# Performance work log

Hardware: AMD Instinct MI355X
Metric: run time of the kernel (lower is better)

Reference implementation:

```python
import jax, jax.numpy as jnp
import numpy as np

N, H, E = 40000, 128, 640000
BN_EPS = 1e-5


def setup_inputs() -> dict:
    key = jax.random.key(0)
    ks = jax.random.split(key, 5)
    x = jax.random.normal(ks[0], (N, H), dtype=jnp.float32)
    edge_index = jax.random.randint(ks[1], (2, E), 0, N, dtype=jnp.int64)
    eps = jnp.zeros((1,), dtype=jnp.float32)
    s = 1.0 / np.sqrt(H)  # torch Linear init scale
    W1 = jax.random.uniform(ks[2], (H, H), jnp.float32, -s, s)
    b1 = jnp.zeros((H,), dtype=jnp.float32)
    W2 = jax.random.uniform(ks[3], (H, H), jnp.float32, -s, s)
    b2 = jnp.zeros((H,), dtype=jnp.float32)
    gamma = jnp.ones((H,), dtype=jnp.float32)
    beta = jnp.zeros((H,), dtype=jnp.float32)
    return {"x": x, "edge_index": edge_index, "eps": eps,
            "W1": W1, "b1": b1, "W2": W2, "b2": b2,
            "gamma": gamma, "beta": beta}


def reference(x, edge_index, eps, W1, b1, W2, b2, gamma, beta):
    src = edge_index[0]
    tgt = edge_index[1]
    # gather source features, scatter-add into target rows: [N, H]
    agg = jax.ops.segment_sum(x[src], tgt, num_segments=x.shape[0])
    out = agg + (1.0 + eps) * x
    # MLP: Linear -> ReLU -> Linear -> BatchNorm1d (train mode) -> ReLU
    h = jax.nn.relu(out @ W1.T + b1)
    h = h @ W2.T + b2
    mean = jnp.mean(h, axis=0)
    var = jnp.mean((h - mean) ** 2, axis=0)  # biased var, as BN uses
    h = (h - mean) * jax.lax.rsqrt(var + BN_EPS) * gamma + beta
    return jax.nn.relu(h)
```

## Files before the change

### kernel.cpp

```cpp
#include <hip/hip_runtime.h>

#define HDIM 128
#define BN_EPS 1e-5f
#define SCAN_BINS 1024
#define NPART 8
#define LSTR 136

typedef short short8 __attribute__((ext_vector_type(8)));
typedef float floatx4 __attribute__((ext_vector_type(4)));

__device__ __forceinline__ unsigned short f2b(float f) {
    union { float f; unsigned u; } v; v.f = f;
    unsigned r = v.u + 0x7FFFu + ((v.u >> 16) & 1u);
    return (unsigned short)(r >> 16);
}

__device__ __forceinline__ float b2f(unsigned short b) {
    union { unsigned u; float f; } v; v.u = (unsigned)b << 16;
    return v.f;
}

__global__ __launch_bounds__(256) void prep_kernel(
    const float* __restrict__ x, unsigned short* __restrict__ xB, long n4,
    const float* __restrict__ W1, const float* __restrict__ W2,
    unsigned short* __restrict__ W1B, unsigned short* __restrict__ W2B,
    const int* __restrict__ eidx, int* __restrict__ hist, int E)
{
    int tid = blockIdx.x * 256 + threadIdx.x;
    int stride = gridDim.x * 256;
    for (long i = tid; i < n4; i += stride) {
        float4 v = ((const float4*)x)[i];
        ushort4 o;
        o.x = f2b(v.x); o.y = f2b(v.y); o.z = f2b(v.z); o.w = f2b(v.w);
        ((ushort4*)xB)[i] = o;
    }
    for (int i = tid; i < HDIM * HDIM; i += stride) {
        W1B[i] = f2b(W1[i]);
        W2B[i] = f2b(W2[i]);
    }
    for (int e = tid; e < E; e += stride) {
        atomicAdd(&hist[eidx[E + e]], 1);
    }
}

__global__ __launch_bounds__(256) void block_scan_kernel(
    const int* __restrict__ hist, int* __restrict__ offsets,
    int* __restrict__ blockSums, float* __restrict__ statSum, int N)
{
    __shared__ int ts[256];
    int b = blockIdx.x, t = threadIdx.x;
    if (b == 0 && t < 2 * HDIM) statSum[t] = 0.f;
    int base = b * SCAN_BINS + t * 4;
    int4 h = make_int4(0, 0, 0, 0);
    if (base + 3 < N) {
        h = *(const int4*)(hist + base);
    } else {
        if (base + 0 < N) h.x = hist[base + 0];
        if (base + 1 < N) h.y = hist[base + 1];
        if (base + 2 < N) h.z = hist[base + 2];
    }
    int s = h.x + h.y + h.z + h.w;
    ts[t] = s;
    __syncthreads();
    for (int off = 1; off < 256; off <<= 1) {
        int v = ts[t];
        int add = (t >= off) ? ts[t - off] : 0;
        __syncthreads();
        ts[t] = v + add;
        __syncthreads();
    }
    int excl = ts[t] - s;
    int4 o;
    o.x = excl;
    o.y = o.x + h.x;
    o.z = o.y + h.y;
    o.w = o.z + h.z;
    if (base + 3 < N) {
        *(int4*)(offsets + base) = o;
    } else {
        if (base + 0 < N) offsets[base + 0] = o.x;
        if (base + 1 < N) offsets[base + 1] = o.y;
        if (base + 2 < N) offsets[base + 2] = o.z;
    }
    if (t == 255) blockSums[b] = ts[255];
}

__global__ __launch_bounds__(256) void scan_finalize_kernel(
    const int* __restrict__ blockSums, int* __restrict__ offsets,
    int* __restrict__ cursor, int N, int NB)
{
    __shared__ int ts[256];
    int b = blockIdx.x, t = threadIdx.x;
    ts[t] = (t < NB) ? blockSums[t] : 0;
    __syncthreads();
    for (int off = 1; off < 256; off <<= 1) {
        int v = ts[t];
        int add = (t >= off) ? ts[t - off] : 0;
        __syncthreads();
        ts[t] = v + add;
        __syncthreads();
    }
    int prefix = (b == 0) ? 0 : ts[b - 1];
    if (b == 0 && t == 0) offsets[N] = ts[NB - 1];
    int base = b * SCAN_BINS + t * 4;
    if (base + 3 < N) {
        int4 o = *(int4*)(offsets + base);
        o.x += prefix; o.y += prefix; o.z += prefix; o.w += prefix;
        *(int4*)(offsets + base) = o;
        *(int4*)(cursor + base) = o;
    } else {
        for (int j = 0; j < 4; j++) {
            int i = base + j;
            if (i < N) {
                int v = offsets[i] + prefix;
                offsets[i] = v;
                cursor[i] = v;
            }
        }
    }
}

__global__ __launch_bounds__(256) void reorder_kernel(
    const int* __restrict__ eidx, int* __restrict__ cursor,
    int* __restrict__ srcSorted, int E, int partSize)
{
    int part = blockIdx.x & (NPART - 1);
    int bi = blockIdx.x >> 3;
    int nb = gridDim.x >> 3;
    int lo = part * partSize;
    int hi = lo + partSize;
    int stride = nb * 256;
    for (int e = bi * 256 + threadIdx.x; e < E; e += stride) {
        int t = eidx[E + e];
        if (t >= lo && t < hi) {
            int pos = atomicAdd(&cursor[t], 1);
            srcSorted[pos] = eidx[e];
        }
    }
}

__global__ __launch_bounds__(256, 6) void mega_kernel(
    const float* __restrict__ x, const unsigned short* __restrict__ xB,
    const int* __restrict__ offsets, const int* __restrict__ srcSorted,
    const float* __restrict__ eps,
    const unsigned short* __restrict__ W1B, const float* __restrict__ b1,
    const unsigned short* __restrict__ W2B, const float* __restrict__ b2,
    float* __restrict__ out, float* __restrict__ statSum,
    float* __restrict__ statSqs, int N)
{
    __shared__ unsigned short sT[64 * LSTR];
    __shared__ float sSum[HDIM];
    __shared__ float sSqs[HDIM];

    int tid = threadIdx.x;
    int rb = blockIdx.x * 64;
    if (tid < HDIM) { sSum[tid] = 0.f; sSqs[tid] = 0.f; }

    float coef = 1.0f + eps[0];
    int tx = tid & 15, ty = tid >> 4;
    for (int g = 0; g < 4; g++) {
        int r = g * 16 + ty;
        int row = rb + r;
        int col = tx * 8;
        float acc[8] = {0.f, 0.f, 0.f, 0.f, 0.f, 0.f, 0.f, 0.f};
        if (row < N) {
            float4 xv0 = *(const float4*)(x + (size_t)row * HDIM + col);
            float4 xv1 = *(const float4*)(x + (size_t)row * HDIM + col + 4);
            acc[0] = coef * xv0.x; acc[1] = coef * xv0.y;
            acc[2] = coef * xv0.z; acc[3] = coef * xv0.w;
            acc[4] = coef * xv1.x; acc[5] = coef * xv1.y;
            acc[6] = coef * xv1.z; acc[7] = coef * xv1.w;
            int beg = offsets[row], end = offsets[row + 1];
            int e = beg;
            for (; e + 3 < end; e += 4) {
                int s0 = srcSorted[e];
                int s1 = srcSorted[e + 1];
                int s2 = srcSorted[e + 2];
                int s3 = srcSorted[e + 3];
                short8 u0 = *(const short8*)(xB + (size_t)s0 * HDIM + col);
                short8 u1 = *(const short8*)(xB + (size_t)s1 * HDIM + col);
                short8 u2 = *(const short8*)(xB + (size_t)s2 * HDIM + col);
                short8 u3 = *(const short8*)(xB + (size_t)s3 * HDIM + col);
                #pragma unroll
                for (int j = 0; j < 8; j++)
                    acc[j] += (b2f((unsigned short)u0[j]) + b2f((unsigned short)u1[j]))
                            + (b2f((unsigned short)u2[j]) + b2f((unsigned short)u3[j]));
            }
            for (; e < end; e++) {
                int s = srcSorted[e];
                short8 u = *(const short8*)(xB + (size_t)s * HDIM + col);
                #pragma unroll
                for (int j = 0; j < 8; j++)
                    acc[j] += b2f((unsigned short)u[j]);
            }
        }
        short8 o;
        #pragma unroll
        for (int j = 0; j < 8; j++) o[j] = (short)f2b(acc[j]);
        *(short8*)(sT + r * LSTR + col) = o;
    }
    __syncthreads();

    int w = tid >> 6;
    int l = tid & 63;
    int m = l & 15, quad = l >> 4;
    unsigned short* myT = sT + w * 16 * LSTR;

    floatx4 acc1[8];
    #pragma unroll
    for (int t = 0; t < 8; t++) acc1[t] = (floatx4){0.f, 0.f, 0.f, 0.f};
    #pragma unroll
    for (int kk = 0; kk < 4; kk++) {
        int k0 = kk * 32 + quad * 8;
        short8 a = *(const short8*)(myT + m * LSTR + k0);
        #pragma unroll
        for (int t = 0; t < 8; t++) {
            short8 bfr = *(const short8*)(W1B + (size_t)(t * 16 + m) * HDIM + k0);
            acc1[t] = __builtin_amdgcn_mfma_f32_16x16x32_bf16(a, bfr, acc1[t], 0, 0, 0);
        }
    }
    #pragma unroll
    for (int t = 0; t < 8; t++) {
        int col = t * 16 + m;
        float bs = b1[col];
        #pragma unroll
        for (int r = 0; r < 4; r++) {
            float v = fmaxf(acc1[t][r] + bs, 0.f);
            myT[(quad * 4 + r) * LSTR + col] = f2b(v);
        }
    }

    floatx4 acc2[8];
    #pragma unroll
    for (int t = 0; t < 8; t++) acc2[t] = (floatx4){0.f, 0.f, 0.f, 0.f};
    #pragma unroll
    for (int kk = 0; kk < 4; kk++) {
        int k0 = kk * 32 + quad * 8;
        short8 a = *(const short8*)(myT + m * LSTR + k0);
        #pragma unroll
        for (int t = 0; t < 8; t++) {
            short8 bfr = *(const short8*)(W2B + (size_t)(t * 16 + m) * HDIM + k0);
            acc2[t] = __builtin_amdgcn_mfma_f32_16x16x32_bf16(a, bfr, acc2[t], 0, 0, 0);
        }
    }
    int row0 = rb + w * 16 + quad * 4;
    #pragma unroll
    for (int t = 0; t < 8; t++) {
        int col = t * 16 + m;
        float bs = b2[col];
        float cs = 0.f, cq = 0.f;
        #pragma unroll
        for (int r = 0; r < 4; r++) {
            int row = row0 + r;
            if (row < N) {
                float v = acc2[t][r] + bs;
                out[(size_t)row * HDIM + col] = v;
                cs += v; cq += v * v;
            }
        }
        cs += __shfl_xor(cs, 16, 64);
        cs += __shfl_xor(cs, 32, 64);
        cq += __shfl_xor(cq, 16, 64);
        cq += __shfl_xor(cq, 32, 64);
        if (quad == 0) {
            atomicAdd(&sSum[col], cs);
            atomicAdd(&sSqs[col], cq);
        }
    }
    __syncthreads();
    if (tid < HDIM) {
        atomicAdd(&statSum[tid], sSum[tid]);
        atomicAdd(&statSqs[tid], sSqs[tid]);
    }
}

__global__ __launch_bounds__(256) void bn_apply_kernel(
    float* __restrict__ out, const float* __restrict__ statSum,
    const float* __restrict__ statSqs, const float* __restrict__ gamma,
    const float* __restrict__ beta, int N, long n4)
{
    __shared__ float sSc[HDIM];
    __shared__ float sSh[HDIM];
    int t = threadIdx.x;
    if (t < HDIM) {
        float invN = 1.0f / (float)N;
        float mean = statSum[t] * invN;
        float var = statSqs[t] * invN - mean * mean;
        float sc = gamma[t] * rsqrtf(var + BN_EPS);
        sSc[t] = sc;
        sSh[t] = beta[t] - mean * sc;
    }
    __syncthreads();
    long stride = (long)gridDim.x * 256;
    for (long i = (long)blockIdx.x * 256 + t; i < n4; i += stride) {
        int cg = (int)(i & 31) * 4;
        float4 v = ((float4*)out)[i];
        v.x = fmaxf(v.x * sSc[cg + 0] + sSh[cg + 0], 0.f);
        v.y = fmaxf(v.y * sSc[cg + 1] + sSh[cg + 1], 0.f);
        v.z = fmaxf(v.z * sSc[cg + 2] + sSh[cg + 2], 0.f);
        v.w = fmaxf(v.w * sSc[cg + 3] + sSh[cg + 3], 0.f);
        ((float4*)out)[i] = v;
    }
}

extern "C" void kernel_launch(void* const* d_in, const int* in_sizes, int n_in,
                              void* d_out, int out_size, void* d_ws, size_t ws_size,
                              hipStream_t stream) {
    const float* x     = (const float*)d_in[0];
    const int*   eidx  = (const int*)d_in[1];
    const float* eps   = (const float*)d_in[2];
    const float* W1    = (const float*)d_in[3];
    const float* b1    = (const float*)d_in[4];
    const float* W2    = (const float*)d_in[5];
    const float* b2    = (const float*)d_in[6];
    const float* gamma = (const float*)d_in[7];
    const float* beta  = (const float*)d_in[8];
    float* out = (float*)d_out;

    int N = in_sizes[0] / HDIM;
    int E = in_sizes[1] / 2;
    size_t NH = (size_t)N * HDIM;
    int NB = (N + SCAN_BINS - 1) / SCAN_BINS;
    int NpadOff = (N + 1 + 3) & ~3;
    int partSize = (N + NPART - 1) / NPART;
    long n4 = (long)NH / 4;

    unsigned short* xB   = (unsigned short*)d_ws;
    unsigned short* W1B  = xB + NH;
    unsigned short* W2B  = W1B + HDIM * HDIM;
    float* statSum = (float*)(W2B + HDIM * HDIM);
    float* statSqs = statSum + HDIM;
    int*   hist    = (int*)(statSqs + HDIM);
    int*   offsets = hist + N;
    int*   cursor  = offsets + NpadOff;
    int*   srcSorted = cursor + N;
    int*   blockSums = srcSorted + E;

    hipMemsetAsync(hist, 0, (size_t)N * sizeof(int), stream);
    prep_kernel<<<1280, 256, 0, stream>>>(x, xB, n4, W1, W2, W1B, W2B, eidx, hist, E);
    block_scan_kernel<<<NB, 256, 0, stream>>>(hist, offsets, blockSums, statSum, N);
    scan_finalize_kernel<<<NB, 256, 0, stream>>>(blockSums, offsets, cursor, N, NB);
    reorder_kernel<<<2048, 256, 0, stream>>>(eidx, cursor, srcSorted, E, partSize);
    int gblocks = (N + 63) / 64;
    mega_kernel<<<gblocks, 256, 0, stream>>>(
        x, xB, offsets, srcSorted, eps, W1B, b1, W2B, b2,
        out, statSum, statSqs, N);
    bn_apply_kernel<<<2048, 256, 0, stream>>>(
        out, statSum, statSqs, gamma, beta, N, n4);
}
```

Before: 215.8 us.

## Split edge gather across two half-warps and halve rows per block

Each block now handles 32 rows instead of 64. Each destination row's edge list is split between two 16-lane halves, which interleave edges and combine their partial sums with a cross-lane shuffle. The MLP stage splits the output columns across wave pairs, so each wave computes 16 rows by 64 columns, with an extra barrier and a separate shared buffer for the hidden activations. The aim is more memory-level parallelism in the gather and more blocks in flight. The cost is more blocks, more per-block atomics for the batch-norm statistics, and each wave reloading the weight fragments.

```diff
diff --git a/kernel.cpp b/kernel.cpp
--- a/kernel.cpp
+++ b/kernel.cpp
@@ -148,35 +148,33 @@
     float* __restrict__ out, float* __restrict__ statSum,
     float* __restrict__ statSqs, int N)
 {
-    __shared__ unsigned short sT[64 * LSTR];
+    __shared__ unsigned short sAgg[32 * LSTR];
+    __shared__ unsigned short sH[32 * LSTR];
     __shared__ float sSum[HDIM];
     __shared__ float sSqs[HDIM];
 
     int tid = threadIdx.x;
-    int rb = blockIdx.x * 64;
+    int rb = blockIdx.x * 32;
     if (tid < HDIM) { sSum[tid] = 0.f; sSqs[tid] = 0.f; }
 
     float coef = 1.0f + eps[0];
-    int tx = tid & 15, ty = tid >> 4;
+    int lane32 = tid & 31;
+    int colgrp = lane32 & 15;
+    int half = lane32 >> 4;
+    int rp = tid >> 5;
+    int col = colgrp * 8;
     for (int g = 0; g < 4; g++) {
-        int r = g * 16 + ty;
+        int r = g * 8 + rp;
         int row = rb + r;
-        int col = tx * 8;
         float acc[8] = {0.f, 0.f, 0.f, 0.f, 0.f, 0.f, 0.f, 0.f};
         if (row < N) {
-            float4 xv0 = *(const float4*)(x + (size_t)row * HDIM + col);
-            float4 xv1 = *(const float4*)(x + (size_t)row * HDIM + col + 4);
-            acc[0] = coef * xv0.x; acc[1] = coef * xv0.y;
-            acc[2] = coef * xv0.z; acc[3] = coef * xv0.w;
-            acc[4] = coef * xv1.x; acc[5] = coef * xv1.y;
-            acc[6] = coef * xv1.z; acc[7] = coef * xv1.w;
             int beg = offsets[row], end = offsets[row + 1];
-            int e = beg;
-            for (; e + 3 < end; e += 4) {
+            int e = beg + half;
+            for (; e + 6 < end; e += 8) {
                 int s0 = srcSorted[e];
-                int s1 = srcSorted[e + 1];
-                int s2 = srcSorted[e + 2];
-                int s3 = srcSorted[e + 3];
+                int s1 = srcSorted[e + 2];
+                int s2 = srcSorted[e + 4];
+                int s3 = srcSorted[e + 6];
                 short8 u0 = *(const short8*)(xB + (size_t)s0 * HDIM + col);
                 short8 u1 = *(const short8*)(xB + (size_t)s1 * HDIM + col);
                 short8 u2 = *(const short8*)(xB + (size_t)s2 * HDIM + col);
@@ -186,75 +184,94 @@
                     acc[j] += (b2f((unsigned short)u0[j]) + b2f((unsigned short)u1[j]))
                             + (b2f((unsigned short)u2[j]) + b2f((unsigned short)u3[j]));
             }
-            for (; e < end; e++) {
+            for (; e < end; e += 2) {
                 int s = srcSorted[e];
                 short8 u = *(const short8*)(xB + (size_t)s * HDIM + col);
                 #pragma unroll
                 for (int j = 0; j < 8; j++)
                     acc[j] += b2f((unsigned short)u[j]);
             }
-        }
-        short8 o;
-        #pragma unroll
-        for (int j = 0; j < 8; j++) o[j] = (short)f2b(acc[j]);
-        *(short8*)(sT + r * LSTR + col) = o;
+            if (half == 0) {
+                float4 xv0 = *(const float4*)(x + (size_t)row * HDIM + col);
+                float4 xv1 = *(const float4*)(x + (size_t)row * HDIM + col + 4);
+                acc[0] += coef * xv0.x; acc[1] += coef * xv0.y;
+                acc[2] += coef * xv0.z; acc[3] += coef * xv0.w;
+                acc[4] += coef * xv1.x; acc[5] += coef * xv1.y;
+                acc[6] += coef * xv1.z; acc[7] += coef * xv1.w;
+            }
+        }
+        #pragma unroll
+        for (int j = 0; j < 8; j++) acc[j] += __shfl_xor(acc[j], 16, 64);
+        if (half == 0) {
+            short8 o;
+            #pragma unroll
+            for (int j = 0; j < 8; j++) o[j] = (short)f2b(acc[j]);
+            *(short8*)(sAgg + r * LSTR + col) = o;
+        }
     }
     __syncthreads();
 
     int w = tid >> 6;
     int l = tid & 63;
     int m = l & 15, quad = l >> 4;
-    unsigned short* myT = sT + w * 16 * LSTR;
-
-    floatx4 acc1[8];
-    #pragma unroll
-    for (int t = 0; t < 8; t++) acc1[t] = (floatx4){0.f, 0.f, 0.f, 0.f};
+    int rowgrp = w & 1;
+    int colhalf = w >> 1;
+    const unsigned short* aSrc = sAgg + rowgrp * 16 * LSTR;
+    unsigned short* hDst = sH + rowgrp * 16 * LSTR;
+
+    floatx4 acc1[4];
+    #pragma unroll
+    for (int t = 0; t < 4; t++) acc1[t] = (floatx4){0.f, 0.f, 0.f, 0.f};
     #pragma unroll
     for (int kk = 0; kk < 4; kk++) {
         int k0 = kk * 32 + quad * 8;
-        short8 a = *(const short8*)(myT + m * LSTR + k0);
-        #pragma unroll
-        for (int t = 0; t < 8; t++) {
-            short8 bfr = *(const short8*)(W1B + (size_t)(t * 16 + m) * HDIM + k0);
+        short8 a = *(const short8*)(aSrc + m * LSTR + k0);
+        #pragma unroll
+        for (int t = 0; t < 4; t++) {
+            int bcol = colhalf * 64 + t * 16 + m;
+            short8 bfr = *(const short8*)(W1B + (size_t)bcol * HDIM + k0);
             acc1[t] = __builtin_amdgcn_mfma_f32_16x16x32_bf16(a, bfr, acc1[t], 0, 0, 0);
         }
     }
     #pragma unroll
-    for (int t = 0; t < 8; t++) {
-        int col = t * 16 + m;
-        float bs = b1[col];
+    for (int t = 0; t < 4; t++) {
+        int colc = colhalf * 64 + t * 16 + m;
+        float bs = b1[colc];
         #pragma unroll
         for (int r = 0; r < 4; r++) {
             float v = fmaxf(acc1[t][r] + bs, 0.f);
-            myT[(quad * 4 + r) * LSTR + col] = f2b(v);
-        }
-    }
-
-    floatx4 acc2[8];
-    #pragma unroll
-    for (int t = 0; t < 8; t++) acc2[t] = (floatx4){0.f, 0.f, 0.f, 0.f};
+            hDst[(quad * 4 + r) * LSTR + colc] = f2b(v);
+        }
+    }
+    __syncthreads();
+
+    const unsigned short* hSrc = sH + rowgrp * 16 * LSTR;
+    floatx4 acc2[4];
+    #pragma unroll
+    for (int t = 0; t < 4; t++) acc2[t] = (floatx4){0.f, 0.f, 0.f, 0.f};
     #pragma unroll
     for (int kk = 0; kk < 4; kk++) {
         int k0 = kk * 32 + quad * 8;
-        short8 a = *(const short8*)(myT + m * LSTR + k0);
-        #pragma unroll
-        for (int t = 0; t < 8; t++) {
-            short8 bfr = *(const short8*)(W2B + (size_t)(t * 16 + m) * HDIM + k0);
+        short8 a = *(const short8*)(hSrc + m * LSTR + k0);
+        #pragma unroll
+        for (int t = 0; t < 4; t++) {
+            int bcol = colhalf * 64 + t * 16 + m;
+            short8 bfr = *(const short8*)(W2B + (size_t)bcol * HDIM + k0);
             acc2[t] = __builtin_amdgcn_mfma_f32_16x16x32_bf16(a, bfr, acc2[t], 0, 0, 0);
         }
     }
-    int row0 = rb + w * 16 + quad * 4;
-    #pragma unroll
-    for (int t = 0; t < 8; t++) {
-        int col = t * 16 + m;
-        float bs = b2[col];
+    int row0 = rb + rowgrp * 16 + quad * 4;
+    #pragma unroll
+    for (int t = 0; t < 4; t++) {
+        int colc = colhalf * 64 + t * 16 + m;
+        float bs = b2[colc];
         float cs = 0.f, cq = 0.f;
         #pragma unroll
         for (int r = 0; r < 4; r++) {
             int row = row0 + r;
             if (row < N) {
                 float v = acc2[t][r] + bs;
-                out[(size_t)row * HDIM + col] = v;
+                out[(size_t)row * HDIM + colc] = v;
                 cs += v; cq += v * v;
             }
         }
@@ -263,8 +280,8 @@
         cq += __shfl_xor(cq, 16, 64);
         cq += __shfl_xor(cq, 32, 64);
         if (quad == 0) {
-            atomicAdd(&sSum[col], cs);
-            atomicAdd(&sSqs[col], cq);
+            atomicAdd(&sSum[colc], cs);
+            atomicAdd(&sSqs[colc], cq);
         }
     }
     __syncthreads();
@@ -341,7 +358,7 @@
     block_scan_kernel<<<NB, 256, 0, stream>>>(hist, offsets, blockSums, statSum, N);
     scan_finalize_kernel<<<NB, 256, 0, stream>>>(blockSums, offsets, cursor, N, NB);
     reorder_kernel<<<2048, 256, 0, stream>>>(eidx, cursor, srcSorted, E, partSize);
-    int gblocks = (N + 63) / 64;
+    int gblocks = (N + 31) / 32;
     mega_kernel<<<gblocks, 256, 0, stream>>>(
         x, xB, offsets, srcSorted, eps, W1B, b1, W2B, b2,
         out, statSum, statSqs, N);
```

New measurement: 224.7 us. 4.1% more time.
